# Performance work log

Hardware: AMD Instinct MI355X
Metric: run time of the kernel (lower is better)

Reference implementation:

```python
import jax, jax.numpy as jnp
import numpy as np

B, T, D = 64, 2048, 256  # batch, seq_len, embedding_dim; units == embedding_dim == D
U = 256


def setup_inputs() -> dict:
    key = jax.random.key(0)
    ks = jax.random.split(key, 8)
    s = 1.0 / np.sqrt(D)
    return {
        "features": jax.random.normal(ks[0], (B, T, D), dtype=jnp.float32),
        "hidden": jax.random.normal(ks[1], (B, D), dtype=jnp.float32),
        "w1_w": jax.random.uniform(ks[2], (U, D), jnp.float32, -s, s),
        "w1_b": jax.random.uniform(ks[3], (U,), jnp.float32, -s, s),
        "w2_w": jax.random.uniform(ks[4], (U, D), jnp.float32, -s, s),
        "w2_b": jax.random.uniform(ks[5], (U,), jnp.float32, -s, s),
        "v_w": jax.random.uniform(ks[6], (1, U), jnp.float32, -s, s),
        "v_b": jax.random.uniform(ks[7], (1,), jnp.float32, -s, s),
    }


def reference(features, hidden, w1_w, w1_b, w2_w, w2_b, v_w, v_b):
    # features: [B, T, D], hidden: [B, D]
    proj = jnp.einsum('btd,ud->btu', features, w1_w) + w1_b  # w1(features)
    hid = jnp.einsum('bd,ud->bu', hidden, w2_w) + w2_b        # w2(hidden)
    score = jnp.einsum('btu,ou->bto', jnp.tanh(proj + hid[:, None, :]), v_w) + v_b  # [B,T,1]
    attn = jax.nn.softmax(score, axis=1)                      # [B,T,1]
    context = jnp.sum(attn * features, axis=1)                # [B,D]
    return context, attn
```

## Files before the change

kernel.cpp:

```cpp
#include <hip/hip_runtime.h>
#include <stdint.h>

#define Bq 64
#define Tq 2048
#define Dq 256
#define Uq 256

typedef __bf16 bf16x8 __attribute__((ext_vector_type(8)));
typedef float f32x4 __attribute__((ext_vector_type(4)));

#define ASTR 1040
#define ABUF (4 * ASTR)
#define BSTR 4128
#define BBUF (4 * BSTR)

__device__ inline unsigned short rne_bf16(float a) {
  unsigned b = __float_as_uint(a);
  return (unsigned short)((b + 0x7FFFu + ((b >> 16) & 1u)) >> 16);
}

__device__ inline float fast_tanh(float x) {
  float e = __expf(2.0f * x);
  return 1.0f - 2.0f * __builtin_amdgcn_rcpf(e + 1.0f);
}

__global__ void k01_prep(const float* __restrict__ w1,
                         unsigned short* __restrict__ w1bf,
                         const float* __restrict__ hidden,
                         const float* __restrict__ w2_w,
                         const float* __restrict__ w2_b,
                         const float* __restrict__ w1_b,
                         float* __restrict__ comb) {
  if (blockIdx.x < 64) {
    int idx = blockIdx.x * 256 + threadIdx.x;
    int i = idx * 4;
    int u = i >> 8;
    int k = i & 255;
    float4 v = *reinterpret_cast<const float4*>(&w1[i]);
    ushort4 h;
    h.x = rne_bf16(v.x);
    h.y = rne_bf16(v.y);
    h.z = rne_bf16(v.z);
    h.w = rne_bf16(v.w);
    int dst = (k >> 3) * (Uq * 8) + u * 8 + (k & 7);
    *reinterpret_cast<ushort4*>(&w1bf[dst]) = h;
  } else {
    int bid = blockIdx.x - 64;
    int b = bid >> 6;
    int wave = threadIdx.x >> 6;
    int lane = threadIdx.x & 63;
    int u = (bid & 63) * 4 + wave;
    const float* h = hidden + b * Dq;
    const float* w = w2_w + u * Dq;
    float sum = 0.f;
#pragma unroll
    for (int i = 0; i < Dq; i += 64) sum += h[lane + i] * w[lane + i];
#pragma unroll
    for (int m = 32; m >= 1; m >>= 1) sum += __shfl_xor(sum, m, 64);
    if (lane == 0) comb[b * Uq + u] = sum + w2_b[u] + w1_b[u];
  }
}

__global__ __launch_bounds__(256) void k2_score(
    const float* __restrict__ feat, const unsigned short* __restrict__ w1bf,
    const float* __restrict__ comb, const float* __restrict__ v_w,
    const float* __restrict__ v_b, float* __restrict__ score) {
  __shared__ char sB[2 * BBUF];
  __shared__ char sA[2 * ABUF];
  __shared__ float scp[4 * 64];
  const int b = blockIdx.y;
  const int t0 = blockIdx.x * 64;
  const int tid = threadIdx.x;
  const int w = tid >> 6;
  const int l = tid & 63;
  const int fr = l & 15;
  const int g = l >> 4;

  const int arow = tid >> 2;
  const int aoct = tid & 3;
  const float* aload = feat + ((size_t)(b * Tq + t0 + arow)) * Dq + aoct * 8;
  char* const awr = sA + aoct * ASTR + arow * 16;

  f32x4 acc[4][4] = {};
  float4 pa[2][2];

  auto issueBdma = [&](int c) {
    char* bbase = sB + (c & 1) * BBUF;
#pragma unroll
    for (int q = 0; q < 4; ++q) {
      int d = w * 4 + q;
      int j = d >> 2;
      int h2 = d & 3;
      const unsigned short* src =
          w1bf + (size_t)(c * 4 + j) * (Uq * 8) + (h2 * 64 + l) * 8;
      __builtin_amdgcn_global_load_lds(
          (const __attribute__((address_space(1))) unsigned int*)src,
          (__attribute__((address_space(3))) unsigned int*)(bbase + j * BSTR +
                                                            h2 * 1024),
          16, 0, 0);
    }
  };
  auto loadA = [&](int c) {
    pa[c & 1][0] = *reinterpret_cast<const float4*>(aload + c * 32);
    pa[c & 1][1] = *reinterpret_cast<const float4*>(aload + c * 32 + 4);
  };
  auto writeA = [&](int c) {
    const float4& v0 = pa[c & 1][0];
    const float4& v1 = pa[c & 1][1];
    uint4 H;
    H.x = rne_bf16(v0.x) | ((unsigned)rne_bf16(v0.y) << 16);
    H.y = rne_bf16(v0.z) | ((unsigned)rne_bf16(v0.w) << 16);
    H.z = rne_bf16(v1.x) | ((unsigned)rne_bf16(v1.y) << 16);
    H.w = rne_bf16(v1.z) | ((unsigned)rne_bf16(v1.w) << 16);
    *reinterpret_cast<uint4*>(awr + (c & 1) * ABUF) = H;
  };
  auto pipeBarrier = [&]() {
    __builtin_amdgcn_sched_barrier(0);
    asm volatile("s_waitcnt vmcnt(2) lgkmcnt(0)" ::: "memory");
    __builtin_amdgcn_s_barrier();
    __builtin_amdgcn_sched_barrier(0);
  };

  issueBdma(0);
  __builtin_amdgcn_sched_barrier(0);
  loadA(0);
  loadA(1);
  __builtin_amdgcn_sched_barrier(0);
  writeA(0);
  pipeBarrier();

#pragma unroll
  for (int c = 0; c < 8; ++c) {
    if (c < 7) {
      issueBdma(c + 1);
      __builtin_amdgcn_sched_barrier(0);
      loadA((c + 2) & 7);
      __builtin_amdgcn_sched_barrier(0);
    }
    const char* bA = sA + (c & 1) * ABUF;
    const char* bB = sB + (c & 1) * BBUF;
    bf16x8 ah[4], bh[4];
#pragma unroll
    for (int mf = 0; mf < 4; ++mf)
      ah[mf] = *reinterpret_cast<const bf16x8*>(bA + g * ASTR +
                                                (mf * 16 + fr) * 16);
#pragma unroll
    for (int nf = 0; nf < 4; ++nf)
      bh[nf] = *reinterpret_cast<const bf16x8*>(
          bB + g * BSTR + (w * 64 + nf * 16 + fr) * 16);
    __builtin_amdgcn_s_setprio(1);
#pragma unroll
    for (int mf = 0; mf < 4; ++mf)
#pragma unroll
      for (int nf = 0; nf < 4; ++nf)
        acc[mf][nf] = __builtin_amdgcn_mfma_f32_16x16x32_bf16(
            ah[mf], bh[nf], acc[mf][nf], 0, 0, 0);
    __builtin_amdgcn_s_setprio(0);
    if (c < 7) {
      writeA(c + 1);
      pipeBarrier();
    }
  }

  float cb[4], vw4[4];
#pragma unroll
  for (int nf = 0; nf < 4; ++nf) {
    int u = w * 64 + nf * 16 + fr;
    cb[nf] = comb[b * Uq + u];
    vw4[nf] = v_w[u];
  }
  float sc[4][4];
#pragma unroll
  for (int mf = 0; mf < 4; ++mf)
#pragma unroll
    for (int r = 0; r < 4; ++r) sc[mf][r] = 0.f;
#pragma unroll
  for (int mf = 0; mf < 4; ++mf)
#pragma unroll
    for (int nf = 0; nf < 4; ++nf)
#pragma unroll
      for (int r = 0; r < 4; ++r)
        sc[mf][r] += vw4[nf] * fast_tanh(acc[mf][nf][r] + cb[nf]);
#pragma unroll
  for (int m = 1; m < 16; m <<= 1)
#pragma unroll
    for (int mf = 0; mf < 4; ++mf)
#pragma unroll
      for (int r = 0; r < 4; ++r) sc[mf][r] += __shfl_xor(sc[mf][r], m, 16);
  __syncthreads();
  if (fr == 0) {
#pragma unroll
    for (int mf = 0; mf < 4; ++mf)
#pragma unroll
      for (int r = 0; r < 4; ++r)
        scp[w * 64 + mf * 16 + g * 4 + r] = sc[mf][r];
  }
  __syncthreads();
  if (tid < 64) {
    float v = scp[tid] + scp[64 + tid] + scp[128 + tid] + scp[192 + tid];
    score[b * Tq + t0 + tid] = v + v_b[0];
  }
}

__global__ void k3_softmax(float* __restrict__ s, float* __restrict__ ctx) {
  int b = blockIdx.x;
  int tid = threadIdx.x;
  const int base = b * Tq;
  ctx[b * Dq + tid] = 0.f;
  float v[8];
  float m = -1e30f;
#pragma unroll
  for (int i = 0; i < 8; ++i) {
    v[i] = s[base + tid + 256 * i];
    m = fmaxf(m, v[i]);
  }
#pragma unroll
  for (int mk = 32; mk >= 1; mk >>= 1) m = fmaxf(m, __shfl_xor(m, mk, 64));
  __shared__ float red[4];
  int wv = tid >> 6, ln = tid & 63;
  if (ln == 0) red[wv] = m;
  __syncthreads();
  m = fmaxf(fmaxf(red[0], red[1]), fmaxf(red[2], red[3]));
  __syncthreads();
  float sum = 0.f;
#pragma unroll
  for (int i = 0; i < 8; ++i) {
    v[i] = __expf(v[i] - m);
    sum += v[i];
  }
#pragma unroll
  for (int mk = 32; mk >= 1; mk >>= 1) sum += __shfl_xor(sum, mk, 64);
  if (ln == 0) red[wv] = sum;
  __syncthreads();
  sum = red[0] + red[1] + red[2] + red[3];
  float inv = 1.f / sum;
#pragma unroll
  for (int i = 0; i < 8; ++i) s[base + tid + 256 * i] = v[i] * inv;
}

__global__ void k4_context(const float* __restrict__ feat,
                           const float* __restrict__ attn,
                           float* __restrict__ ctx) {
  int b = blockIdx.x;
  int ts = blockIdx.y;
  int d = threadIdx.x;
  const int t0 = ts * 256;
  const float* f = feat + ((size_t)(b * Tq + t0)) * Dq + d;
  const float* a = attn + b * Tq + t0;
  float acc = 0.f;
#pragma unroll 8
  for (int t = 0; t < 256; ++t) acc += a[t] * f[(size_t)t * Dq];
  atomicAdd(&ctx[b * Dq + d], acc);
}

extern "C" void kernel_launch(void* const* d_in, const int* in_sizes, int n_in,
                              void* d_out, int out_size, void* d_ws,
                              size_t ws_size, hipStream_t stream) {
  const float* feat   = (const float*)d_in[0];
  const float* hidden = (const float*)d_in[1];
  const float* w1_w   = (const float*)d_in[2];
  const float* w1_b   = (const float*)d_in[3];
  const float* w2_w   = (const float*)d_in[4];
  const float* w2_b   = (const float*)d_in[5];
  const float* v_w    = (const float*)d_in[6];
  const float* v_b    = (const float*)d_in[7];

  float* ctx  = (float*)d_out;
  float* attn = ctx + Bq * Dq;
  float* comb = (float*)d_ws;
  unsigned short* w1bf = (unsigned short*)(comb + Bq * Uq);

  k01_prep<<<64 + Bq * 64, 256, 0, stream>>>(w1_w, w1bf, hidden, w2_w, w2_b,
                                             w1_b, comb);
  k2_score<<<dim3(Tq / 64, Bq), 256, 0, stream>>>(feat, w1bf, comb, v_w, v_b,
                                                  attn);
  k3_softmax<<<Bq, 256, 0, stream>>>(attn, ctx);
  k4_context<<<dim3(Bq, 8), 256, 0, stream>>>(feat, attn, ctx);
}
```

Before: 73.81 us.

## Fuse context accumulation into score kernel with online-softmax partials

The score kernel now computes a per-tile max and exp weights, then accumulates a partial context vector over its 64 timesteps while the feature tile is likely still cache-resident. A new combine kernel rescales the tile partials by the global softmax max and sum. This removes the separate context kernel, which re-read the full 128MB feature tensor, and its atomics. In exchange it adds partial-buffer traffic and extra tail work in the score kernel.

```diff
diff --git a/kernel.cpp b/kernel.cpp
--- a/kernel.cpp
+++ b/kernel.cpp
@@ -5,6 +5,7 @@
 #define Tq 2048
 #define Dq 256
 #define Uq 256
+#define NTILE 32
 
 typedef __bf16 bf16x8 __attribute__((ext_vector_type(8)));
 typedef float f32x4 __attribute__((ext_vector_type(4)));
@@ -64,12 +65,15 @@
 __global__ __launch_bounds__(256) void k2_score(
     const float* __restrict__ feat, const unsigned short* __restrict__ w1bf,
     const float* __restrict__ comb, const float* __restrict__ v_w,
-    const float* __restrict__ v_b, float* __restrict__ score) {
+    const float* __restrict__ v_b, float* __restrict__ score,
+    float* __restrict__ pm, float* __restrict__ partc) {
   __shared__ char sB[2 * BBUF];
   __shared__ char sA[2 * ABUF];
   __shared__ float scp[4 * 64];
+  __shared__ float ebuf[64];
   const int b = blockIdx.y;
-  const int t0 = blockIdx.x * 64;
+  const int tile = blockIdx.x;
+  const int t0 = tile * 64;
   const int tid = threadIdx.x;
   const int w = tid >> 6;
   const int l = tid & 63;
@@ -197,16 +201,29 @@
   }
   __syncthreads();
   if (tid < 64) {
-    float v = scp[tid] + scp[64 + tid] + scp[128 + tid] + scp[192 + tid];
-    score[b * Tq + t0 + tid] = v + v_b[0];
-  }
-}
-
-__global__ void k3_softmax(float* __restrict__ s, float* __restrict__ ctx) {
+    float v =
+        scp[tid] + scp[64 + tid] + scp[128 + tid] + scp[192 + tid] + v_b[0];
+    score[b * Tq + t0 + tid] = v;
+    float m = v;
+#pragma unroll
+    for (int mk = 32; mk >= 1; mk >>= 1) m = fmaxf(m, __shfl_xor(m, mk, 64));
+    ebuf[tid] = __expf(v - m);
+    if (tid == 0) pm[b * NTILE + tile] = m;
+  }
+  __syncthreads();
+  {
+    const float* frow = feat + (size_t)(b * Tq + t0) * Dq + tid;
+    float cd = 0.f;
+#pragma unroll 8
+    for (int t = 0; t < 64; ++t) cd += ebuf[t] * frow[(size_t)t * Dq];
+    partc[((size_t)b * NTILE + tile) * Dq + tid] = cd;
+  }
+}
+
+__global__ void k3_softmax(float* __restrict__ s, float* __restrict__ stats) {
   int b = blockIdx.x;
   int tid = threadIdx.x;
   const int base = b * Tq;
-  ctx[b * Dq + tid] = 0.f;
   float v[8];
   float m = -1e30f;
 #pragma unroll
@@ -236,21 +253,28 @@
   float inv = 1.f / sum;
 #pragma unroll
   for (int i = 0; i < 8; ++i) s[base + tid + 256 * i] = v[i] * inv;
-}
-
-__global__ void k4_context(const float* __restrict__ feat,
-                           const float* __restrict__ attn,
+  if (tid == 0) {
+    stats[b * 2 + 0] = m;
+    stats[b * 2 + 1] = inv;
+  }
+}
+
+__global__ void k5_combine(const float* __restrict__ partc,
+                           const float* __restrict__ pm,
+                           const float* __restrict__ stats,
                            float* __restrict__ ctx) {
   int b = blockIdx.x;
-  int ts = blockIdx.y;
   int d = threadIdx.x;
-  const int t0 = ts * 256;
-  const float* f = feat + ((size_t)(b * Tq + t0)) * Dq + d;
-  const float* a = attn + b * Tq + t0;
-  float acc = 0.f;
-#pragma unroll 8
-  for (int t = 0; t < 256; ++t) acc += a[t] * f[(size_t)t * Dq];
-  atomicAdd(&ctx[b * Dq + d], acc);
+  const float M = stats[b * 2 + 0];
+  const float invS = stats[b * 2 + 1];
+  __shared__ float wgt[NTILE];
+  if (d < NTILE) wgt[d] = __expf(pm[b * NTILE + d] - M);
+  __syncthreads();
+  float s = 0.f;
+#pragma unroll
+  for (int j = 0; j < NTILE; ++j)
+    s += wgt[j] * partc[((size_t)b * NTILE + j) * Dq + d];
+  ctx[b * Dq + d] = s * invS;
 }
 
 extern "C" void kernel_launch(void* const* d_in, const int* in_sizes, int n_in,
@@ -269,11 +293,14 @@
   float* attn = ctx + Bq * Dq;
   float* comb = (float*)d_ws;
   unsigned short* w1bf = (unsigned short*)(comb + Bq * Uq);
+  float* partc = (float*)(w1bf + Uq * Dq);
+  float* pm    = partc + (size_t)Bq * NTILE * Dq;
+  float* stats = pm + Bq * NTILE;
 
   k01_prep<<<64 + Bq * 64, 256, 0, stream>>>(w1_w, w1bf, hidden, w2_w, w2_b,
                                              w1_b, comb);
-  k2_score<<<dim3(Tq / 64, Bq), 256, 0, stream>>>(feat, w1bf, comb, v_w, v_b,
-                                                  attn);
-  k3_softmax<<<Bq, 256, 0, stream>>>(attn, ctx);
-  k4_context<<<dim3(Bq, 8), 256, 0, stream>>>(feat, attn, ctx);
-}
+  k2_score<<<dim3(NTILE, Bq), 256, 0, stream>>>(feat, w1bf, comb, v_w, v_b,
+                                                attn, pm, partc);
+  k3_softmax<<<Bq, 256, 0, stream>>>(attn, stats);
+  k5_combine<<<Bq, 256, 0, stream>>>(partc, pm, stats, ctx);
+}
```

Measured after the change: 68.84 us. 6.7% less time.
